# Optimization experiments

Hardware: AMD Instinct MI355X
Metric: run time of the kernel (lower is better)

## Reference

```python
import jax, jax.numpy as jnp
import numpy as np

B, T, C = 4, 4096, 1024
H, CS = 16, 128
D = C // H
EPS = 1e-5

def _ln(x, g, b):
    m = jnp.mean(x, axis=-1, keepdims=True)
    v = jnp.var(x, axis=-1, keepdims=True)
    return (x - m) * jax.lax.rsqrt(v + EPS) * g + b

def setup_inputs() -> dict:
    key = jax.random.key(0)
    ks = jax.random.split(key, 12)
    s_c = 1.0 / np.sqrt(C)
    s_2d = 1.0 / np.sqrt(2 * D)
    return {
        "x": jax.random.normal(ks[0], (B, T, C), jnp.float32),
        "mark_W": jax.random.normal(ks[1], (C, C), jnp.float32) * s_c,
        "mark_b": jnp.zeros((C,), jnp.float32),
        "gate_W": jax.random.normal(ks[2], (C, C), jnp.float32) * s_c,
        "gate_b": jnp.zeros((C,), jnp.float32),
        "carry_g": jnp.ones((D,), jnp.float32),
        "carry_b": jnp.zeros((D,), jnp.float32),
        "card_g": jnp.ones((D,), jnp.float32),
        "card_b": jnp.zeros((D,), jnp.float32),
        "ho1_W": jax.random.normal(ks[3], (2 * D, 2 * D), jnp.float32) * s_2d,
        "ho1_b": jnp.zeros((2 * D,), jnp.float32),
        "ho2_W": jax.random.normal(ks[4], (2 * D, D), jnp.float32) * s_2d,
        "ho2_b": jnp.zeros((D,), jnp.float32),
        "proj_W": jax.random.normal(ks[5], (C, C), jnp.float32) * s_c * 0.02,
        "proj_b": jnp.zeros((C,), jnp.float32),
        "ln_g": jnp.ones((C,), jnp.float32),
        "ln_b": jnp.zeros((C,), jnp.float32),
    }

def reference(x, mark_W, mark_b, gate_W, gate_b, carry_g, carry_b,
              card_g, card_b, ho1_W, ho1_b, ho2_W, ho2_b,
              proj_W, proj_b, ln_g, ln_b):
    b, t, c = x.shape
    nc = t // CS  # T chosen divisible by chunk_size -> pad_len = 0
    pm = x @ mark_W + mark_b                       # [B,T,C]
    gates = jax.nn.sigmoid(x @ gate_W + gate_b)    # [B,T,C]

    def chunks(a):  # [B,T,C] -> [B,H,nc,CS,D]
        return a.reshape(b, nc, CS, H, D).transpose(0, 3, 1, 2, 4)

    x_h = chunks(x)
    gm = chunks(gates) * chunks(pm)                # gated marks
    lcm = jnp.cumsum(gm, axis=3)                   # local prefix sum within chunk
    chunk_sums = lcm[:, :, :, -1, :]               # [B,H,nc,D]
    carry_cum = jnp.cumsum(chunk_sums, axis=2)
    carries = jnp.concatenate(
        [jnp.zeros((b, H, 1, D), x.dtype), carry_cum[:, :, :-1, :]], axis=2)
    nrm_carry = _ln(carries, carry_g, carry_b)[:, :, :, None, :]  # [B,H,nc,1,D]
    mwc = lcm + nrm_carry                          # marks with carry
    cards_local = jnp.concatenate([nrm_carry, mwc[:, :, :, :-1, :]], axis=3)
    cards = _ln(cards_local, card_g, card_b)
    comb = jnp.concatenate([x_h, cards], axis=-1)  # [B,H,nc,CS,2D]
    h = jax.nn.gelu(comb @ ho1_W + ho1_b, approximate=False)
    ho = h @ ho2_W + ho2_b                         # [B,H,nc,CS,D]
    out = ho.transpose(0, 2, 3, 1, 4).reshape(b, t, c)
    out = out @ proj_W + proj_b
    out = _ln(out, ln_g, ln_b)
    return x + out
```

## Files before the change

kernel.cpp:

```cpp
#include <hip/hip_runtime.h>
#include <hip/hip_bf16.h>

typedef __bf16 bf16_t;
typedef __attribute__((ext_vector_type(8))) __bf16 bf16x8;
typedef __attribute__((ext_vector_type(4))) __bf16 bf16x4;
typedef __attribute__((ext_vector_type(4))) float f32x4;

static constexpr int Bn = 4, Tn = 4096, Cn = 1024, Hn = 16, CSn = 128, Dn = 64, NCn = 32;

#define DEVINL __device__ __forceinline__

DEVINL float wsum64(float v) {
  v += __shfl_xor(v, 32, 64);
  v += __shfl_xor(v, 16, 64);
  v += __shfl_xor(v, 8, 64);
  v += __shfl_xor(v, 4, 64);
  v += __shfl_xor(v, 2, 64);
  v += __shfl_xor(v, 1, 64);
  return v;
}

DEVINL float gelu_f(float v) {
  float x = v * 0.70710678f;
  float ax = fabsf(x);
  float t = 1.f / (1.f + 0.3275911f * ax);
  float poly = t * (0.254829592f +
               t * (-0.284496736f +
               t * (1.421413741f +
               t * (-1.453152027f +
               t * 1.061405429f))));
  float e = __expf(-ax * ax);
  float erfax = 1.f - poly * e;
  float erfx = copysignf(erfax, x);
  return 0.5f * v * (1.f + erfx);
}

DEVINL void gld16(const bf16_t* g, bf16_t* l) {
  __builtin_amdgcn_global_load_lds(
      (const __attribute__((address_space(1))) unsigned int*)(g),
      (__attribute__((address_space(3))) unsigned int*)(l), 16, 0, 0);
}

__global__ __launch_bounds__(256) void k_xbf(const float* __restrict__ in,
                                             bf16_t* __restrict__ out) {
  int i = blockIdx.x * 256 + threadIdx.x;
  float4 a = *reinterpret_cast<const float4*>(in + (size_t)i * 8);
  float4 b = *reinterpret_cast<const float4*>(in + (size_t)i * 8 + 4);
  bf16x8 o = {(bf16_t)a.x, (bf16_t)a.y, (bf16_t)a.z, (bf16_t)a.w,
              (bf16_t)b.x, (bf16_t)b.y, (bf16_t)b.z, (bf16_t)b.w};
  *reinterpret_cast<bf16x8*>(out + (size_t)i * 8) = o;
}

__global__ void k_transpose(const float* __restrict__ in, bf16_t* __restrict__ out,
                            int rows, int cols) {
  __shared__ float tile[64][65];
  int c0 = blockIdx.x * 64, r0 = blockIdx.y * 64;
  int tx = threadIdx.x & 63, ty = threadIdx.x >> 6;
#pragma unroll
  for (int i = ty; i < 64; i += 4)
    tile[i][tx] = in[(size_t)(r0 + i) * cols + c0 + tx];
  __syncthreads();
#pragma unroll
  for (int i = ty; i < 64; i += 4)
    out[(size_t)(c0 + i) * rows + r0 + tx] = (bf16_t)tile[tx][i];
}

__global__ __launch_bounds__(256, 3) void k_dualgemm_gm(
    const bf16_t* __restrict__ X, const bf16_t* __restrict__ Wtm,
    const bf16_t* __restrict__ Wtg, const float* __restrict__ bm,
    const float* __restrict__ bg, bf16_t* __restrict__ lcm,
    float* __restrict__ csum) {
  constexpr int K = Cn, N = Cn;
  constexpr int GP = 68;
  __shared__ __align__(16) bf16_t L[16384];
  __shared__ float tot[4][64];
  int tid = threadIdx.x;
  int Lb = blockIdx.x;
  int xcd = Lb & 7, jj = Lb >> 3;
  int nb = jj & 15, mb = xcd + 8 * (jj >> 4);
  int m0 = mb * 128, n0 = nb * 64;
  int wave = tid >> 6, lane = tid & 63;
  int wm = wave >> 1, wn = wave & 1;
  int lr = lane & 15, lk = lane >> 4;
  int rl = lane >> 2;
  int cl = (lane & 3) * 8;
  f32x4 accP[4][2] = {};
  f32x4 accG[4][2] = {};

  const bf16_t* Xb = X + (size_t)m0 * K;
  const bf16_t* Wmb = Wtm + (size_t)n0 * K;
  const bf16_t* Wgb = Wtg + (size_t)n0 * K;
  bf16_t* LA = L;
  bf16_t* LBm = L + 8192;
  bf16_t* LBg = L + 12288;

#define STAGE3(buf, kt)                                                    \
  {                                                                        \
    _Pragma("unroll")                                                      \
    for (int c = 0; c < 2; ++c) {                                          \
      int ch = wave * 2 + c;                                               \
      gld16(Xb + (size_t)(ch * 16 + rl) * K + (kt) * 32 + cl,              \
            LA + (buf) * 4096 + ch * 512);                                 \
    }                                                                      \
    size_t gob = (size_t)(wave * 16 + rl) * K + (kt) * 32 + cl;            \
    gld16(Wmb + gob, LBm + (buf) * 2048 + wave * 512);                     \
    gld16(Wgb + gob, LBg + (buf) * 2048 + wave * 512);                     \
  }

  STAGE3(0, 0);
  __syncthreads();
  int cur = 0;
  for (int kt = 0; kt < 32; ++kt) {
    if (kt < 31) STAGE3(cur ^ 1, kt + 1);
    bf16x8 af[4], bmf[2], bgf[2];
#pragma unroll
    for (int i = 0; i < 4; ++i)
      af[i] = *reinterpret_cast<const bf16x8*>(
          &LA[cur * 4096 + (wm * 64 + i * 16 + lr) * 32 + lk * 8]);
#pragma unroll
    for (int j = 0; j < 2; ++j) {
      bmf[j] = *reinterpret_cast<const bf16x8*>(
          &LBm[cur * 2048 + (wn * 32 + j * 16 + lr) * 32 + lk * 8]);
      bgf[j] = *reinterpret_cast<const bf16x8*>(
          &LBg[cur * 2048 + (wn * 32 + j * 16 + lr) * 32 + lk * 8]);
    }
#pragma unroll
    for (int i = 0; i < 4; ++i)
#pragma unroll
      for (int j = 0; j < 2; ++j) {
        accP[i][j] = __builtin_amdgcn_mfma_f32_16x16x32_bf16(af[i], bmf[j], accP[i][j], 0, 0, 0);
        accG[i][j] = __builtin_amdgcn_mfma_f32_16x16x32_bf16(af[i], bgf[j], accG[i][j], 0, 0, 0);
      }
    __syncthreads();
    cur ^= 1;
  }
#undef STAGE3

  bf16_t* G = L;
#pragma unroll
  for (int j = 0; j < 2; ++j) {
    int col = wn * 32 + j * 16 + lr;
    float bmv = bm[n0 + col], bgv = bg[n0 + col];
#pragma unroll
    for (int i = 0; i < 4; ++i) {
      int rbase = wm * 64 + i * 16 + lk * 4;
#pragma unroll
      for (int r = 0; r < 4; ++r) {
        float p = accP[i][j][r] + bmv;
        float g = accG[i][j][r] + bgv;
        float s = 1.f / (1.f + __expf(-g));
        G[(rbase + r) * GP + col] = (bf16_t)(s * p);
      }
    }
  }
  __syncthreads();
  {
    int col = tid & 63;
    int q = tid >> 6;
    float lsum = 0.f;
#pragma unroll 8
    for (int r = 0; r < 32; ++r)
      lsum += (float)G[(q * 32 + r) * GP + col];
    tot[q][col] = lsum;
    __syncthreads();
    float run = 0.f;
#pragma unroll
    for (int qq = 0; qq < 3; ++qq)
      if (qq < q) run += tot[qq][col];
    int gc = n0 + col;
    size_t obase = (size_t)(m0 + q * 32) * N + gc;
#pragma unroll 8
    for (int r = 0; r < 32; ++r) {
      run += (float)G[(q * 32 + r) * GP + col];
      lcm[obase + (size_t)r * N] = (bf16_t)run;
    }
    if (q == 3) {
      int bb = m0 >> 12;
      int ci = (m0 >> 7) & 31;
      csum[(((size_t)bb * Hn + (gc >> 6)) * NCn + ci) * 64 + (gc & 63)] = run;
    }
  }
}

__global__ __launch_bounds__(64) void k_carry_ln(const float* __restrict__ csum,
                                                 float* __restrict__ ncar,
                                                 const float* __restrict__ g,
                                                 const float* __restrict__ be) {
  int bh = blockIdx.x;
  int d = threadIdx.x;
  float gd = g[d], bd = be[d];
  float run = 0.f;
  for (int ci = 0; ci < NCn; ++ci) {
    float v = run;
    run += csum[((size_t)bh * NCn + ci) * 64 + d];
    float m = wsum64(v) * (1.f / 64.f);
    float dv = v - m;
    float var = wsum64(dv * dv) * (1.f / 64.f);
    ncar[((size_t)bh * NCn + ci) * 64 + d] = dv * rsqrtf(var + 1e-5f) * gd + bd;
  }
}

__global__ __launch_bounds__(256) void k_cards(
    const bf16_t* __restrict__ lcm, const float* __restrict__ ncar,
    const float* __restrict__ cg, const float* __restrict__ cb,
    bf16_t* __restrict__ cards) {
  int blk = blockIdx.x;
  int ci = blk & 31, bh = blk >> 5;
  int h = bh & 15, b = bh >> 4;
  int wave = threadIdx.x >> 6, lane = threadIdx.x & 63;
  int lg = lane >> 3;
  int le = lane & 7;
  int d0 = le * 8;
  size_t xrow0 = (size_t)(b * Tn + ci * CSn);
  const float* np = ncar + ((size_t)bh * NCn + ci) * 64 + d0;
  float ncv[8], ggv[8], bbv[8];
#pragma unroll
  for (int e = 0; e < 8; ++e) {
    ncv[e] = np[e];
    ggv[e] = cg[d0 + e];
    bbv[e] = cb[d0 + e];
  }
#pragma unroll
  for (int it = 0; it < 4; ++it) {
    int pr = wave * 32 + it * 8 + lg;
    float v[8];
    if (pr > 0) {
      bf16x8 lv = *reinterpret_cast<const bf16x8*>(
          lcm + (xrow0 + pr - 1) * Cn + h * Dn + d0);
#pragma unroll
      for (int e = 0; e < 8; ++e) v[e] = (float)lv[e] + ncv[e];
    } else {
#pragma unroll
      for (int e = 0; e < 8; ++e) v[e] = ncv[e];
    }
    float s = 0.f;
#pragma unroll
    for (int e = 0; e < 8; ++e) s += v[e];
    s += __shfl_xor(s, 1, 64);
    s += __shfl_xor(s, 2, 64);
    s += __shfl_xor(s, 4, 64);
    float mean = s * (1.f / 64.f);
    float q = 0.f;
#pragma unroll
    for (int e = 0; e < 8; ++e) { float dv = v[e] - mean; q += dv * dv; }
    q += __shfl_xor(q, 1, 64);
    q += __shfl_xor(q, 2, 64);
    q += __shfl_xor(q, 4, 64);
    float rs = rsqrtf(q * (1.f / 64.f) + 1e-5f);
    bf16x8 o;
#pragma unroll
    for (int e = 0; e < 8; ++e)
      o[e] = (bf16_t)((v[e] - mean) * rs * ggv[e] + bbv[e]);
    *reinterpret_cast<bf16x8*>(cards + ((size_t)blk * CSn + pr) * 64 + d0) = o;
  }
}

__global__ __launch_bounds__(256, 4) void k_ho_fused(
    const bf16_t* __restrict__ X, const bf16_t* __restrict__ cards,
    const bf16_t* __restrict__ W1t, const float* __restrict__ b1,
    const bf16_t* __restrict__ W2t, const float* __restrict__ b2,
    bf16_t* __restrict__ ho) {
  __shared__ __align__(16) bf16_t S[128 * 136];
  int tid = threadIdx.x;
  int blk = blockIdx.x;
  int ci = blk & 31, bh = blk >> 5;
  int h = bh & 15, b = bh >> 4;
  int wave = tid >> 6, lane = tid & 63;
  int wm = wave >> 1, wn = wave & 1;
  int lr = lane & 15, lk = lane >> 4;
  size_t xrow0 = (size_t)(b * Tn + ci * CSn);

  {
    const bf16_t* cbase = cards + (size_t)blk * CSn * 64;
#pragma unroll
    for (int c = 0; c < 4; ++c) {
      int row = wave * 32 + c * 8 + (lane >> 3);
      int c16 = (lane & 7) ^ (row & 7);
      gld16(cbase + (size_t)row * 64 + c16 * 8, S + (wave * 32 + c * 8) * 64);
    }
  }
  bf16x8 xf0[4], xf1[4];
#pragma unroll
  for (int i = 0; i < 4; ++i) {
    const bf16_t* xr = X + (xrow0 + wm * 64 + i * 16 + lr) * Cn + h * Dn + lk * 8;
    xf0[i] = *reinterpret_cast<const bf16x8*>(xr);
    xf1[i] = *reinterpret_cast<const bf16x8*>(xr + 32);
  }
  __syncthreads();

  f32x4 acc[4][4] = {};
#pragma unroll
  for (int ks = 0; ks < 4; ++ks) {
    bf16x8 af[4], bfr[4];
#pragma unroll
    for (int i = 0; i < 4; ++i) {
      if (ks == 0)      af[i] = xf0[i];
      else if (ks == 1) af[i] = xf1[i];
      else {
        int row = wm * 64 + i * 16 + lr;
        int c16 = ((ks - 2) * 4 + lk) ^ (lr & 7);
        af[i] = *reinterpret_cast<const bf16x8*>(&S[row * 64 + c16 * 8]);
      }
    }
#pragma unroll
    for (int j = 0; j < 4; ++j)
      bfr[j] = *reinterpret_cast<const bf16x8*>(
          W1t + (size_t)(wn * 64 + j * 16 + lr) * 128 + ks * 32 + lk * 8);
#pragma unroll
    for (int i = 0; i < 4; ++i)
#pragma unroll
      for (int j = 0; j < 4; ++j)
        acc[i][j] = __builtin_amdgcn_mfma_f32_16x16x32_bf16(af[i], bfr[j], acc[i][j], 0, 0, 0);
  }
  __syncthreads();
#pragma unroll
  for (int j = 0; j < 4; ++j) {
    int col = wn * 64 + j * 16 + lr;
    float bv = b1[col];
#pragma unroll
    for (int i = 0; i < 4; ++i) {
      int rbase = wm * 64 + i * 16 + lk * 4;
#pragma unroll
      for (int r = 0; r < 4; ++r)
        S[(rbase + r) * 136 + col] = (bf16_t)gelu_f(acc[i][j][r] + bv);
    }
  }
  __syncthreads();
  f32x4 acc2[2][4] = {};
#pragma unroll
  for (int ks = 0; ks < 4; ++ks) {
    bf16x8 af[2], bfr[4];
#pragma unroll
    for (int i = 0; i < 2; ++i)
      af[i] = *reinterpret_cast<const bf16x8*>(
          &S[(wave * 32 + i * 16 + lr) * 136 + ks * 32 + lk * 8]);
#pragma unroll
    for (int j = 0; j < 4; ++j)
      bfr[j] = *reinterpret_cast<const bf16x8*>(
          W2t + (size_t)(j * 16 + lr) * 128 + ks * 32 + lk * 8);
#pragma unroll
    for (int i = 0; i < 2; ++i)
#pragma unroll
      for (int j = 0; j < 4; ++j)
        acc2[i][j] = __builtin_amdgcn_mfma_f32_16x16x32_bf16(af[i], bfr[j], acc2[i][j], 0, 0, 0);
  }
#pragma unroll
  for (int j = 0; j < 4; ++j) {
    int dd = j * 16 + lr;
    float bv = b2[dd];
#pragma unroll
    for (int i = 0; i < 2; ++i) {
      int pbase = wave * 32 + i * 16 + lk * 4;
#pragma unroll
      for (int r = 0; r < 4; ++r)
        ho[(xrow0 + pbase + r) * Cn + h * Dn + dd] = (bf16_t)(acc2[i][j][r] + bv);
    }
  }
}

__global__ __launch_bounds__(256, 2) void k_gemm_bt(
    const bf16_t* __restrict__ A, const bf16_t* __restrict__ Wt,
    const float* __restrict__ bias, bf16_t* __restrict__ out) {
  constexpr int K = Cn, N = Cn;
  __shared__ __align__(16) bf16_t L[4][128 * 32];
  int tid = threadIdx.x;
  int Lb = blockIdx.x + 8 * blockIdx.y;
  int xcd = Lb & 7, jj = Lb >> 3;
  int nb = jj & 7, mb = xcd + 8 * (jj >> 3);
  int m0 = mb * 128, n0 = nb * 128;
  int wave = tid >> 6, lane = tid & 63;
  int wm = wave >> 1, wn = wave & 1;
  int lr = lane & 15, lk = lane >> 4;
  int rl = lane >> 2, cl = (lane & 3) * 8;
  f32x4 acc[4][4] = {};
  const bf16_t* Ab = A + (size_t)m0 * K;
  const bf16_t* Wb = Wt + (size_t)n0 * K;

#define STAGE2(buf, kt)                                                    \
  {                                                                        \
    _Pragma("unroll")                                                      \
    for (int c = 0; c < 2; ++c) {                                          \
      int ch = wave * 2 + c;                                               \
      size_t go = (size_t)(ch * 16 + rl) * K + (kt) * 32 + cl;             \
      int lo = ch * 512;                                                   \
      gld16(Ab + go, &L[0 + (buf)][lo]);                                   \
      gld16(Wb + go, &L[2 + (buf)][lo]);                                   \
    }                                                                      \
  }

  STAGE2(0, 0);
  __syncthreads();
  int cur = 0;
  for (int kt = 0; kt < 32; ++kt) {
    if (kt < 31) STAGE2(cur ^ 1, kt + 1);
    bf16x8 af[4], bfr[4];
#pragma unroll
    for (int i = 0; i < 4; ++i)
      af[i] = *reinterpret_cast<const bf16x8*>(&L[0 + cur][(wm * 64 + i * 16 + lr) * 32 + lk * 8]);
#pragma unroll
    for (int j = 0; j < 4; ++j)
      bfr[j] = *reinterpret_cast<const bf16x8*>(&L[2 + cur][(wn * 64 + j * 16 + lr) * 32 + lk * 8]);
#pragma unroll
    for (int i = 0; i < 4; ++i)
#pragma unroll
      for (int j = 0; j < 4; ++j)
        acc[i][j] = __builtin_amdgcn_mfma_f32_16x16x32_bf16(af[i], bfr[j], acc[i][j], 0, 0, 0);
    __syncthreads();
    cur ^= 1;
  }
#undef STAGE2
#pragma unroll
  for (int j = 0; j < 4; ++j) {
    int col = n0 + wn * 64 + j * 16 + lr;
    float bv = bias[col];
#pragma unroll
    for (int i = 0; i < 4; ++i) {
      int rbase = m0 + wm * 64 + i * 16 + lk * 4;
#pragma unroll
      for (int r = 0; r < 4; ++r)
        out[(size_t)(rbase + r) * N + col] = (bf16_t)(acc[i][j][r] + bv);
    }
  }
}

__global__ __launch_bounds__(256) void k_ln_residual(
    const bf16_t* __restrict__ pre, const bf16_t* __restrict__ Xb,
    const float* __restrict__ g, const float* __restrict__ be,
    float* __restrict__ out) {
  int row = blockIdx.x, t = threadIdx.x;
  size_t base = (size_t)row * Cn + t * 4;
  bf16x4 pv4 = *reinterpret_cast<const bf16x4*>(pre + base);
  float v0 = (float)pv4[0], v1 = (float)pv4[1], v2 = (float)pv4[2], v3 = (float)pv4[3];
  float s = v0 + v1 + v2 + v3;
  float q = v0 * v0 + v1 * v1 + v2 * v2 + v3 * v3;
  s = wsum64(s);
  q = wsum64(q);
  __shared__ float red[8];
  int wv = t >> 6, ln = t & 63;
  if (ln == 0) { red[wv] = s; red[4 + wv] = q; }
  __syncthreads();
  float tot = red[0] + red[1] + red[2] + red[3];
  float totq = red[4] + red[5] + red[6] + red[7];
  float mean = tot * (1.f / 1024.f);
  float var = totq * (1.f / 1024.f) - mean * mean;
  float rs = rsqrtf(fmaxf(var, 0.f) + 1e-5f);
  bf16x4 xv4 = *reinterpret_cast<const bf16x4*>(Xb + base);
  float4 gv = *reinterpret_cast<const float4*>(g + t * 4);
  float4 bv = *reinterpret_cast<const float4*>(be + t * 4);
  float4 o;
  o.x = (v0 - mean) * rs * gv.x + bv.x + (float)xv4[0];
  o.y = (v1 - mean) * rs * gv.y + bv.y + (float)xv4[1];
  o.z = (v2 - mean) * rs * gv.z + bv.z + (float)xv4[2];
  o.w = (v3 - mean) * rs * gv.w + bv.w + (float)xv4[3];
  *reinterpret_cast<float4*>(out + base) = o;
}

extern "C" void kernel_launch(void* const* d_in, const int* in_sizes, int n_in,
                              void* d_out, int out_size, void* d_ws, size_t ws_size,
                              hipStream_t stream) {
  const float* x       = (const float*)d_in[0];
  const float* mark_W  = (const float*)d_in[1];
  const float* mark_b  = (const float*)d_in[2];
  const float* gate_W  = (const float*)d_in[3];
  const float* gate_b  = (const float*)d_in[4];
  const float* carry_g = (const float*)d_in[5];
  const float* carry_b = (const float*)d_in[6];
  const float* card_g  = (const float*)d_in[7];
  const float* card_b  = (const float*)d_in[8];
  const float* ho1_W   = (const float*)d_in[9];
  const float* ho1_b   = (const float*)d_in[10];
  const float* ho2_W   = (const float*)d_in[11];
  const float* ho2_b   = (const float*)d_in[12];
  const float* proj_W  = (const float*)d_in[13];
  const float* proj_b  = (const float*)d_in[14];
  const float* ln_g    = (const float*)d_in[15];
  const float* ln_b    = (const float*)d_in[16];
  float* out = (float*)d_out;

  char* ws = (char*)d_ws;
  bf16_t* xbf    = (bf16_t*)(ws + 0);
  bf16_t* gm     = (bf16_t*)(ws + 33554432);
  bf16_t* cards  = (bf16_t*)(ws + 67108864);
  bf16_t* outpre = (bf16_t*)(ws + 67108864);
  bf16_t* hobuf  = (bf16_t*)(ws + 100663296);
  float*  csum   = (float*)(ws + 134217728);
  float*  ncar   = (float*)(ws + 134742016);
  bf16_t* wtm    = (bf16_t*)(ws + 135266304);
  bf16_t* wtg    = (bf16_t*)(ws + 137363456);
  bf16_t* wtp    = (bf16_t*)(ws + 139460608);
  bf16_t* wt1    = (bf16_t*)(ws + 141557760);
  bf16_t* wt2    = (bf16_t*)(ws + 141590528);

  k_xbf<<<8192, 256, 0, stream>>>(x, xbf);
  k_transpose<<<dim3(16, 16), 256, 0, stream>>>(mark_W, wtm, 1024, 1024);
  k_transpose<<<dim3(16, 16), 256, 0, stream>>>(gate_W, wtg, 1024, 1024);
  k_transpose<<<dim3(16, 16), 256, 0, stream>>>(proj_W, wtp, 1024, 1024);
  k_transpose<<<dim3(2, 2),   256, 0, stream>>>(ho1_W, wt1, 128, 128);
  k_transpose<<<dim3(1, 2),   256, 0, stream>>>(ho2_W, wt2, 128, 64);

  k_dualgemm_gm<<<2048, 256, 0, stream>>>(xbf, wtm, wtg, mark_b, gate_b, gm, csum);
  k_carry_ln<<<64, 64, 0, stream>>>(csum, ncar, carry_g, carry_b);
  k_cards<<<2048, 256, 0, stream>>>(gm, ncar, card_g, card_b, cards);
  k_ho_fused<<<2048, 256, 0, stream>>>(xbf, cards, wt1, ho1_b, wt2, ho2_b, hobuf);
  k_gemm_bt<<<dim3(8, 128), 256, 0, stream>>>(hobuf, wtp, proj_b, outpre);
  k_ln_residual<<<16384, 256, 0, stream>>>(outpre, xbf, ln_g, ln_b, out);
}
```

Baseline: 269.5 us.

## Fuse carry layernorm into cards kernel, load cards to registers, retune launch bounds

The separate serial carry-layernorm kernel is removed. Each cards block now recomputes its chunk's carry prefix by summing earlier chunk sums and applies the layernorm inline, which drops one launch and a low-parallelism serial step at the cost of redundant O(nc) reads per block. The ho kernel now loads its card fragments straight from global memory into registers instead of staging them through LDS, which removes one barrier but raises register pressure. Occupancy hints for k_ho_fused (4→3) and k_gemm_bt (2→3) are also changed.

```diff
diff --git a/kernel.cpp b/kernel.cpp
--- a/kernel.cpp
+++ b/kernel.cpp
@@ -182,26 +182,9 @@
   }
 }
 
-__global__ __launch_bounds__(64) void k_carry_ln(const float* __restrict__ csum,
-                                                 float* __restrict__ ncar,
-                                                 const float* __restrict__ g,
-                                                 const float* __restrict__ be) {
-  int bh = blockIdx.x;
-  int d = threadIdx.x;
-  float gd = g[d], bd = be[d];
-  float run = 0.f;
-  for (int ci = 0; ci < NCn; ++ci) {
-    float v = run;
-    run += csum[((size_t)bh * NCn + ci) * 64 + d];
-    float m = wsum64(v) * (1.f / 64.f);
-    float dv = v - m;
-    float var = wsum64(dv * dv) * (1.f / 64.f);
-    ncar[((size_t)bh * NCn + ci) * 64 + d] = dv * rsqrtf(var + 1e-5f) * gd + bd;
-  }
-}
-
 __global__ __launch_bounds__(256) void k_cards(
-    const bf16_t* __restrict__ lcm, const float* __restrict__ ncar,
+    const bf16_t* __restrict__ lcm, const float* __restrict__ csum,
+    const float* __restrict__ crg, const float* __restrict__ crb,
     const float* __restrict__ cg, const float* __restrict__ cb,
     bf16_t* __restrict__ cards) {
   int blk = blockIdx.x;
@@ -212,13 +195,37 @@
   int le = lane & 7;
   int d0 = le * 8;
   size_t xrow0 = (size_t)(b * Tn + ci * CSn);
-  const float* np = ncar + ((size_t)bh * NCn + ci) * 64 + d0;
+
+  float cv[8] = {0.f, 0.f, 0.f, 0.f, 0.f, 0.f, 0.f, 0.f};
+  for (int k = 0; k < ci; ++k) {
+    const float* cp = csum + ((size_t)bh * NCn + k) * 64 + d0;
+    float4 a = *reinterpret_cast<const float4*>(cp);
+    float4 c = *reinterpret_cast<const float4*>(cp + 4);
+    cv[0] += a.x; cv[1] += a.y; cv[2] += a.z; cv[3] += a.w;
+    cv[4] += c.x; cv[5] += c.y; cv[6] += c.z; cv[7] += c.w;
+  }
   float ncv[8], ggv[8], bbv[8];
-#pragma unroll
-  for (int e = 0; e < 8; ++e) {
-    ncv[e] = np[e];
-    ggv[e] = cg[d0 + e];
-    bbv[e] = cb[d0 + e];
+  {
+    float s = 0.f;
+#pragma unroll
+    for (int e = 0; e < 8; ++e) s += cv[e];
+    s += __shfl_xor(s, 1, 64);
+    s += __shfl_xor(s, 2, 64);
+    s += __shfl_xor(s, 4, 64);
+    float mean = s * (1.f / 64.f);
+    float q = 0.f;
+#pragma unroll
+    for (int e = 0; e < 8; ++e) { float dv = cv[e] - mean; q += dv * dv; }
+    q += __shfl_xor(q, 1, 64);
+    q += __shfl_xor(q, 2, 64);
+    q += __shfl_xor(q, 4, 64);
+    float rs = rsqrtf(q * (1.f / 64.f) + 1e-5f);
+#pragma unroll
+    for (int e = 0; e < 8; ++e) {
+      ncv[e] = (cv[e] - mean) * rs * crg[d0 + e] + crb[d0 + e];
+      ggv[e] = cg[d0 + e];
+      bbv[e] = cb[d0 + e];
+    }
   }
 #pragma unroll
   for (int it = 0; it < 4; ++it) {
@@ -255,7 +262,7 @@
   }
 }
 
-__global__ __launch_bounds__(256, 4) void k_ho_fused(
+__global__ __launch_bounds__(256, 3) void k_ho_fused(
     const bf16_t* __restrict__ X, const bf16_t* __restrict__ cards,
     const bf16_t* __restrict__ W1t, const float* __restrict__ b1,
     const bf16_t* __restrict__ W2t, const float* __restrict__ b2,
@@ -270,38 +277,21 @@
   int lr = lane & 15, lk = lane >> 4;
   size_t xrow0 = (size_t)(b * Tn + ci * CSn);
 
-  {
-    const bf16_t* cbase = cards + (size_t)blk * CSn * 64;
-#pragma unroll
-    for (int c = 0; c < 4; ++c) {
-      int row = wave * 32 + c * 8 + (lane >> 3);
-      int c16 = (lane & 7) ^ (row & 7);
-      gld16(cbase + (size_t)row * 64 + c16 * 8, S + (wave * 32 + c * 8) * 64);
-    }
-  }
-  bf16x8 xf0[4], xf1[4];
+  bf16x8 af[4][4];
 #pragma unroll
   for (int i = 0; i < 4; ++i) {
     const bf16_t* xr = X + (xrow0 + wm * 64 + i * 16 + lr) * Cn + h * Dn + lk * 8;
-    xf0[i] = *reinterpret_cast<const bf16x8*>(xr);
-    xf1[i] = *reinterpret_cast<const bf16x8*>(xr + 32);
-  }
-  __syncthreads();
+    af[0][i] = *reinterpret_cast<const bf16x8*>(xr);
+    af[1][i] = *reinterpret_cast<const bf16x8*>(xr + 32);
+    const bf16_t* cr = cards + ((size_t)blk * CSn + wm * 64 + i * 16 + lr) * 64 + lk * 8;
+    af[2][i] = *reinterpret_cast<const bf16x8*>(cr);
+    af[3][i] = *reinterpret_cast<const bf16x8*>(cr + 32);
+  }
 
   f32x4 acc[4][4] = {};
 #pragma unroll
   for (int ks = 0; ks < 4; ++ks) {
-    bf16x8 af[4], bfr[4];
-#pragma unroll
-    for (int i = 0; i < 4; ++i) {
-      if (ks == 0)      af[i] = xf0[i];
-      else if (ks == 1) af[i] = xf1[i];
-      else {
-        int row = wm * 64 + i * 16 + lr;
-        int c16 = ((ks - 2) * 4 + lk) ^ (lr & 7);
-        af[i] = *reinterpret_cast<const bf16x8*>(&S[row * 64 + c16 * 8]);
-      }
-    }
+    bf16x8 bfr[4];
 #pragma unroll
     for (int j = 0; j < 4; ++j)
       bfr[j] = *reinterpret_cast<const bf16x8*>(
@@ -310,9 +300,8 @@
     for (int i = 0; i < 4; ++i)
 #pragma unroll
       for (int j = 0; j < 4; ++j)
-        acc[i][j] = __builtin_amdgcn_mfma_f32_16x16x32_bf16(af[i], bfr[j], acc[i][j], 0, 0, 0);
-  }
-  __syncthreads();
+        acc[i][j] = __builtin_amdgcn_mfma_f32_16x16x32_bf16(af[ks][i], bfr[j], acc[i][j], 0, 0, 0);
+  }
 #pragma unroll
   for (int j = 0; j < 4; ++j) {
     int col = wn * 64 + j * 16 + lr;
@@ -329,10 +318,10 @@
   f32x4 acc2[2][4] = {};
 #pragma unroll
   for (int ks = 0; ks < 4; ++ks) {
-    bf16x8 af[2], bfr[4];
+    bf16x8 ha[2], bfr[4];
 #pragma unroll
     for (int i = 0; i < 2; ++i)
-      af[i] = *reinterpret_cast<const bf16x8*>(
+      ha[i] = *reinterpret_cast<const bf16x8*>(
           &S[(wave * 32 + i * 16 + lr) * 136 + ks * 32 + lk * 8]);
 #pragma unroll
     for (int j = 0; j < 4; ++j)
@@ -342,7 +331,7 @@
     for (int i = 0; i < 2; ++i)
 #pragma unroll
       for (int j = 0; j < 4; ++j)
-        acc2[i][j] = __builtin_amdgcn_mfma_f32_16x16x32_bf16(af[i], bfr[j], acc2[i][j], 0, 0, 0);
+        acc2[i][j] = __builtin_amdgcn_mfma_f32_16x16x32_bf16(ha[i], bfr[j], acc2[i][j], 0, 0, 0);
   }
 #pragma unroll
   for (int j = 0; j < 4; ++j) {
@@ -358,7 +347,7 @@
   }
 }
 
-__global__ __launch_bounds__(256, 2) void k_gemm_bt(
+__global__ __launch_bounds__(256, 3) void k_gemm_bt(
     const bf16_t* __restrict__ A, const bf16_t* __restrict__ Wt,
     const float* __restrict__ bias, bf16_t* __restrict__ out) {
   constexpr int K = Cn, N = Cn;
@@ -484,7 +473,6 @@
   bf16_t* outpre = (bf16_t*)(ws + 67108864);
   bf16_t* hobuf  = (bf16_t*)(ws + 100663296);
   float*  csum   = (float*)(ws + 134217728);
-  float*  ncar   = (float*)(ws + 134742016);
   bf16_t* wtm    = (bf16_t*)(ws + 135266304);
   bf16_t* wtg    = (bf16_t*)(ws + 137363456);
   bf16_t* wtp    = (bf16_t*)(ws + 139460608);
@@ -499,8 +487,7 @@
   k_transpose<<<dim3(1, 2),   256, 0, stream>>>(ho2_W, wt2, 128, 64);
 
   k_dualgemm_gm<<<2048, 256, 0, stream>>>(xbf, wtm, wtg, mark_b, gate_b, gm, csum);
-  k_carry_ln<<<64, 64, 0, stream>>>(csum, ncar, carry_g, carry_b);
-  k_cards<<<2048, 256, 0, stream>>>(gm, ncar, card_g, card_b, cards);
+  k_cards<<<2048, 256, 0, stream>>>(gm, csum, carry_g, carry_b, card_g, card_b, cards);
   k_ho_fused<<<2048, 256, 0, stream>>>(xbf, cards, wt1, ho1_b, wt2, ho2_b, hobuf);
   k_gemm_bt<<<dim3(8, 128), 256, 0, stream>>>(hobuf, wtp, proj_b, outpre);
   k_ln_residual<<<16384, 256, 0, stream>>>(outpre, xbf, ln_g, ln_b, out);
```

Measured after the change: 278.7 us. +3.4%, slower.
